# Kernel optimization log

Hardware: AMD Instinct MI355X
Metric: run time of the kernel (lower is better)

Reference implementation:

```python
import jax, jax.numpy as jnp
import numpy as np

NUM_TASKS = 150
ACT_DIM = 4
ENC_DIM = 256
EMB_DIM = 32
HEAD_HID = 128
B, H, W = 256, 128, 128


def _conv(x, w, b):
    # x: NCHW, w: OIHW, stride 2, padding 1 (torch Conv2d semantics)
    y = jax.lax.conv_general_dilated(x, w, window_strides=(2, 2),
                                     padding=((1, 1), (1, 1)),
                                     dimension_numbers=('NCHW', 'OIHW', 'NCHW'))
    return y + b[None, :, None, None]


def setup_inputs() -> dict:
    key = jax.random.key(0)
    ks = iter(jax.random.split(key, 32))
    s = 0.05
    d = {
        'images': jax.random.normal(next(ks), (B, 3, H, W), jnp.float32),
        'proprioception': jax.random.normal(next(ks), (B, 7), jnp.float32),
        'task_ids': jax.random.randint(next(ks), (B,), 0, NUM_TASKS, jnp.int32),
        # vision encoder convs (OIHW)
        'c1_w': jax.random.normal(next(ks), (64, 3, 3, 3), jnp.float32) * s,
        'c1_b': jnp.zeros((64,), jnp.float32),
        'c2_w': jax.random.normal(next(ks), (128, 64, 3, 3), jnp.float32) * s,
        'c2_b': jnp.zeros((128,), jnp.float32),
        'c3_w': jax.random.normal(next(ks), (256, 128, 3, 3), jnp.float32) * s,
        'c3_b': jnp.zeros((256,), jnp.float32),
        # proprioception encoder (weights stored as [in, out])
        'p1_w': jax.random.normal(next(ks), (7, 64), jnp.float32) * s,
        'p1_b': jnp.zeros((64,), jnp.float32),
        'p2_w': jax.random.normal(next(ks), (64, 64), jnp.float32) * s,
        'p2_b': jnp.zeros((64,), jnp.float32),
        # shared-encoder fusion MLP (320 -> 256 -> 256)
        'f1_w': jax.random.normal(next(ks), (256 + 64, ENC_DIM), jnp.float32) * s,
        'f1_b': jnp.zeros((ENC_DIM,), jnp.float32),
        'f2_w': jax.random.normal(next(ks), (ENC_DIM, ENC_DIM), jnp.float32) * s,
        'f2_b': jnp.zeros((ENC_DIM,), jnp.float32),
        # task embedding table
        'task_emb': jax.random.normal(next(ks), (NUM_TASKS, EMB_DIM), jnp.float32) * s,
        # policy-level fusion (288 -> 256), dropout is identity at inference
        'g_w': jax.random.normal(next(ks), (ENC_DIM + EMB_DIM, ENC_DIM), jnp.float32) * s,
        'g_b': jnp.zeros((ENC_DIM,), jnp.float32),
        # stacked task-specific heads [num_tasks, in, out]
        'h1_w': jax.random.normal(next(ks), (NUM_TASKS, ENC_DIM, HEAD_HID), jnp.float32) * s,
        'h1_b': jnp.zeros((NUM_TASKS, HEAD_HID), jnp.float32),
        'h2_w': jax.random.normal(next(ks), (NUM_TASKS, HEAD_HID, HEAD_HID), jnp.float32) * s,
        'h2_b': jnp.zeros((NUM_TASKS, HEAD_HID), jnp.float32),
        'h3_w': jax.random.normal(next(ks), (NUM_TASKS, HEAD_HID, ACT_DIM), jnp.float32) * s,
        'h3_b': jnp.zeros((NUM_TASKS, ACT_DIM), jnp.float32),
    }
    return d


def reference(images, proprioception, task_ids,
              c1_w, c1_b, c2_w, c2_b, c3_w, c3_b,
              p1_w, p1_b, p2_w, p2_b,
              f1_w, f1_b, f2_w, f2_b,
              task_emb, g_w, g_b,
              h1_w, h1_b, h2_w, h2_b, h3_w, h3_b):
    relu = jax.nn.relu
    # vision encoder: 3 strided convs + global avg pool (AdaptiveAvgPool2d(1,1))
    v = relu(_conv(images, c1_w, c1_b))
    v = relu(_conv(v, c2_w, c2_b))
    v = relu(_conv(v, c3_w, c3_b))
    v = jnp.mean(v, axis=(2, 3))                      # [B, 256]
    # proprioception encoder (no final ReLU)
    p = relu(proprioception @ p1_w + p1_b) @ p2_w + p2_b  # [B, 64]
    # shared fusion
    f = relu(jnp.concatenate([v, p], axis=1) @ f1_w + f1_b)
    f = relu(f @ f2_w + f2_b)                         # [B, 256]
    # task embedding + policy fusion (dropout = identity in eval)
    e = task_emb[task_ids]                            # [B, 32]
    z = relu(jnp.concatenate([f, e], axis=1) @ g_w + g_b)  # [B, 256]
    # routed task heads: gather per-sample expert params, batched matmuls
    a = relu(jnp.einsum('bd,bdh->bh', z, h1_w[task_ids]) + h1_b[task_ids])
    a = relu(jnp.einsum('bd,bdh->bh', a, h2_w[task_ids]) + h2_b[task_ids])
    a = jnp.einsum('bd,bdh->bh', a, h3_w[task_ids]) + h3_b[task_ids]  # [B, 4]
    return a
```

## Files before the change

kernel.cpp:

```cpp
#include <hip/hip_runtime.h>
#include <hip/hip_bf16.h>

#define DIV_UP(a,b) (((a)+(b)-1)/(b))

typedef __attribute__((ext_vector_type(8))) short short8;
typedef __attribute__((ext_vector_type(4))) float f32x4;

__device__ __forceinline__ ushort bf16_bits(float x) {
    return __builtin_bit_cast(ushort, __float2bfloat16(x));
}

__device__ __forceinline__ void gload_lds16(const ushort* g, ushort* l) {
    __builtin_amdgcn_global_load_lds(
        (const __attribute__((address_space(1))) void*)g,
        (__attribute__((address_space(3))) void*)l, 16, 0, 0);
}

__global__ __launch_bounds__(256) void halo_zero_kernel(
    uint4* __restrict__ act1, uint4* __restrict__ act2,
    float4* __restrict__ vbuf) {
    const int b = blockIdx.x, tid = threadIdx.x;
    const uint4 z = {0u, 0u, 0u, 0u};
    uint4* a1 = act1 + (size_t)b * 33800;
    for (int i = tid; i < 520; i += 256) a1[i] = z;
    for (int i = tid; i < 512; i += 256) {
        int r = (i >> 3) + 1;
        a1[r * 520 + (i & 7)] = z;
    }
    uint4* a2 = act2 + (size_t)b * 17424;
    for (int i = tid; i < 528; i += 256) a2[i] = z;
    for (int i = tid; i < 512; i += 256) {
        int r = (i >> 4) + 1;
        a2[r * 528 + (i & 15)] = z;
    }
    int idx = b * 256 + tid;
    float4 zf = {0.f, 0.f, 0.f, 0.f};
    if (idx < 16384) vbuf[idx] = zf;
}

__global__ void repack_w1_kernel(const float* __restrict__ src,
                                 __hip_bfloat16* __restrict__ dst) {
    int t = blockIdx.x * blockDim.x + threadIdx.x;
    if (t >= 2048) return;
    int k  = t & 31;
    int oc = t >> 5;
    dst[t] = (k < 27) ? __float2bfloat16(src[oc * 27 + k])
                      : __float2bfloat16(0.f);
}

__global__ void repack_w_kernel(const float* __restrict__ src,
                                __hip_bfloat16* __restrict__ dst, int O, int C) {
    int t = blockIdx.x * blockDim.x + threadIdx.x;
    if (t >= O * C * 9) return;
    int e   = t & 7;
    int r   = t >> 3;
    int n   = r % O;
    int q   = r / O;
    int SEG = C >> 3;
    int sg  = q % SEG;
    int tap = q / SEG;
    dst[t] = __float2bfloat16(src[(n * C + sg * 8 + e) * 9 + tap]);
}

__global__ __launch_bounds__(256) void conv1_mfma_kernel(
    const float* __restrict__ in,
    const __hip_bfloat16* __restrict__ wB,
    const float* __restrict__ bias,
    __hip_bfloat16* __restrict__ out) {
    const int tid  = threadIdx.x;
    const int lane = tid & 63;
    const int wv   = tid >> 6;
    const int l15  = lane & 15;
    const int quad = lane >> 4;
    const int tile = blockIdx.x;
    const int b    = blockIdx.y;
    const int oh0  = tile << 2;

    __shared__ __align__(16) char smem[30208];
    float*  sx = (float*)smem;
    ushort* Al = (ushort*)(smem + 13824);

    const float* ip  = in + (size_t)b * 3 * 128 * 128;
    const int    ih0 = 2 * oh0 - 1;

#pragma unroll
    for (int it = 0; it < 4; ++it) {
        int e = (it << 8) + tid;
        if (e < 864) {
            int q = e >> 5, k = e & 31;
            int c = q / 9, r = q - c * 9;
            int row = ih0 + r;
            if (row < 0) row = 0;
            gload_lds16((const ushort*)(ip + c * 16384 + row * 128 + k * 4),
                        (ushort*)smem + (size_t)e * 8);
        }
    }
    __syncthreads();

    const int px = tid, ohl = px >> 6, ow = px & 63;
    union { uint4 u4[4]; ushort us[32]; } rowv;
#pragma unroll
    for (int c = 0; c < 3; ++c)
#pragma unroll
        for (int kh = 0; kh < 3; ++kh) {
            const bool rok = (ih0 + 2 * ohl + kh) >= 0;
            const float* srow = sx + (c * 9 + 2 * ohl + kh) * 128;
#pragma unroll
            for (int kw = 0; kw < 3; ++kw) {
                int iw = 2 * ow + kw - 1;
                bool ok = rok && (iw >= 0);
                float x = srow[iw < 0 ? 0 : iw];
                rowv.us[c * 9 + kh * 3 + kw] = bf16_bits(ok ? x : 0.f);
            }
        }
#pragma unroll
    for (int k = 27; k < 32; ++k) rowv.us[k] = 0;
#pragma unroll
    for (int q = 0; q < 4; ++q)
        *(uint4*)(Al + px * 32 + (((q ^ (px >> 1)) & 3) << 3)) = rowv.u4[q];

    short8 af[4], bf[4];
#pragma unroll
    for (int i = 0; i < 4; ++i)
        af[i] = __builtin_bit_cast(short8,
            *(const uint4*)(wB + ((i * 16 + l15) * 32 + quad * 8)));

    __syncthreads();

#pragma unroll
    for (int j = 0; j < 4; ++j) {
        int p = wv * 64 + j * 16 + l15;
        bf[j] = __builtin_bit_cast(short8,
            *(const uint4*)(Al + p * 32 + (((quad ^ (p >> 1)) & 3) << 3)));
    }
    f32x4 acc[4][4];
#pragma unroll
    for (int i = 0; i < 4; ++i)
#pragma unroll
        for (int j = 0; j < 4; ++j)
            acc[i][j] = __builtin_amdgcn_mfma_f32_16x16x32_bf16(
                af[i], bf[j], (f32x4){0.f, 0.f, 0.f, 0.f}, 0, 0, 0);

    float4 bv[4];
#pragma unroll
    for (int i = 0; i < 4; ++i)
        bv[i] = *(const float4*)(bias + i * 16 + quad * 4);

    __hip_bfloat16* ob = out + (((size_t)b * 65 + oh0 + 1) * 65 + 1) * 64;
#pragma unroll
    for (int j = 0; j < 4; ++j) {
        const int oww = j * 16 + l15;
        __hip_bfloat16* op = ob + ((size_t)(wv * 65) + oww) * 64 + quad * 4;
#pragma unroll
        for (int i = 0; i < 4; ++i) {
            union { uint2 u2; ushort us[4]; } pk;
#pragma unroll
            for (int r = 0; r < 4; ++r)
                pk.us[r] = bf16_bits(
                    fmaxf(acc[i][j][r] + ((const float*)&bv[i])[r], 0.f));
            *(uint2*)(op + i * 16) = pk.u2;
        }
    }
}

__global__ __launch_bounds__(256, 2) void conv2_gemm_kernel(
    const __hip_bfloat16* __restrict__ act,
    const __hip_bfloat16* __restrict__ wtB,
    const float* __restrict__ bias,
    __hip_bfloat16* __restrict__ out) {
    const int tid  = threadIdx.x;
    const int lane = tid & 63;
    const int w    = tid >> 6;
    const int l15  = lane & 15;
    const int quad = lane >> 4;
    const int per  = gridDim.x >> 3;
    const int Mt   = (blockIdx.x & 7) * per + (blockIdx.x >> 3);
    const int bimg = Mt >> 3;
    const int oh0  = (Mt & 7) << 2;

    __shared__ __align__(16) char smem[77824];
    ushort* As = (ushort*)smem;
    ushort* Cs = (ushort*)smem;

    f32x4 acc[4][4];
#pragma unroll
    for (int i = 0; i < 4; ++i)
#pragma unroll
        for (int j = 0; j < 4; ++j) acc[i][j] = (f32x4){0.f, 0.f, 0.f, 0.f};

    const int wm = (w & 1) << 6;
    const int wn = (w >> 1) << 6;
    const size_t abase = ((size_t)(bimg * 65 + 2 * oh0)) * 65 * 64;
    const ushort* ap = (const ushort*)act;

#pragma unroll
    for (int it = 0; it < 19; ++it) {
        int c  = (it << 8) + tid;
        int p  = c >> 3;
        int t  = c & 7;
        int h  = t >> 2;
        int ss = (t & 3) ^ ((p >> 1) & 3);
        gload_lds16(ap + abase + (size_t)p * 64 + h * 32 + ss * 8,
                    As + (size_t)c * 8);
    }
    __syncthreads();

    for (int h = 0; h < 2; ++h) {
#pragma unroll
        for (int tap = 0; tap < 9; ++tap) {
            const int kh = tap / 3, kw = tap - kh * 3;
            short8 af[4], bf[4];
#pragma unroll
            for (int i = 0; i < 4; ++i) {
                int ml = wm + i * 16 + l15;
                int p  = ((ml >> 5) * 2 + kh) * 65 + ((ml & 31) * 2 + kw);
                af[i] = __builtin_bit_cast(short8,
                    *(const uint4*)(As + p * 64 + h * 32 +
                                    (((quad ^ (p >> 1)) & 3) << 3)));
            }
#pragma unroll
            for (int j = 0; j < 4; ++j)
                bf[j] = __builtin_bit_cast(short8,
                    *(const uint4*)(wtB +
                        ((size_t)((tap * 8 + h * 4 + quad) * 128) +
                         wn + j * 16 + l15) * 8));
#pragma unroll
            for (int i = 0; i < 4; ++i)
#pragma unroll
                for (int j = 0; j < 4; ++j)
                    acc[i][j] = __builtin_amdgcn_mfma_f32_16x16x32_bf16(
                        af[i], bf[j], acc[i][j], 0, 0, 0);
        }
    }

    __syncthreads();
#pragma unroll
    for (int j = 0; j < 4; ++j) {
        int n = wn + j * 16 + l15;
        float bv = bias[n];
#pragma unroll
        for (int i = 0; i < 4; ++i)
#pragma unroll
            for (int r = 0; r < 4; ++r) {
                int ml = wm + i * 16 + quad * 4 + r;
                Cs[ml * 132 + n] = bf16_bits(fmaxf(acc[i][j][r] + bv, 0.f));
            }
    }
    __syncthreads();
#pragma unroll
    for (int q = 0; q < 16; ++q) {
        int c   = tid + 256 * q;
        int row = c >> 5;
        int off = c & 31;
        uint2 val = *(const uint2*)(Cs + row * 132 + off * 4);
        int m  = (Mt << 7) + row;
        int b  = m >> 10;
        int rr = m & 1023;
        int oh = rr >> 5;
        int ow = rr & 31;
        size_t pix = ((size_t)(b * 33 + oh + 1) * 33 + (ow + 1));
        *(uint2*)(out + pix * 128 + off * 4) = val;
    }
}

__global__ __launch_bounds__(256, 2) void conv3_gemm_pool_kernel(
    const __hip_bfloat16* __restrict__ act,
    const __hip_bfloat16* __restrict__ wtB,
    const float* __restrict__ bias,
    float* __restrict__ v ) {
    const int tid  = threadIdx.x;
    const int lane = tid & 63;
    const int w    = tid >> 6;
    const int l15  = lane & 15;
    const int quad = lane >> 4;
    const int per  = gridDim.x >> 3;
    const int Mt   = (blockIdx.x & 7) * per + (blockIdx.x >> 3);
    const int bimg = Mt >> 2;
    const int oh0  = (Mt & 3) << 2;

    __shared__ __align__(16) char smem[77824];
    ushort* As   = (ushort*)smem;
    float*  sred = (float*)smem;

    f32x4 acc[4][4];
#pragma unroll
    for (int i = 0; i < 4; ++i)
#pragma unroll
        for (int j = 0; j < 4; ++j) acc[i][j] = (f32x4){0.f, 0.f, 0.f, 0.f};

    const int wn = w << 6;
    const size_t abase = ((size_t)(bimg * 33 + 2 * oh0)) * 33 * 128;
    const ushort* ap = (const ushort*)act;

#pragma unroll
    for (int it = 0; it < 19; ++it) {
        int c  = (it << 8) + tid;
        int p  = c >> 4;
        int t  = c & 15;
        int h  = t >> 3;
        int ss = (t & 7) ^ ((p >> 1) & 7);
        gload_lds16(ap + abase + (size_t)p * 128 + h * 64 + ss * 8,
                    As + (size_t)c * 8);
    }
    __syncthreads();

    for (int h = 0; h < 2; ++h) {
#pragma unroll 1
        for (int tap = 0; tap < 9; ++tap) {
            const int kh = tap / 3, kw = tap - kh * 3;
#pragma unroll
            for (int ks = 0; ks < 2; ++ks) {
                short8 af[4], bf[4];
                const int sl = ks * 4 + quad;
#pragma unroll
                for (int i = 0; i < 4; ++i) {
                    int p = (i * 2 + kh) * 33 + l15 * 2 + kw;
                    af[i] = __builtin_bit_cast(short8,
                        *(const uint4*)(As + p * 128 + h * 64 +
                                        (((sl ^ (p >> 1)) & 7) << 3)));
                }
#pragma unroll
                for (int j = 0; j < 4; ++j)
                    bf[j] = __builtin_bit_cast(short8,
                        *(const uint4*)(wtB +
                            ((size_t)((tap * 16 + h * 8 + sl) * 256) +
                             wn + j * 16 + l15) * 8));
#pragma unroll
                for (int i = 0; i < 4; ++i)
#pragma unroll
                    for (int j = 0; j < 4; ++j)
                        acc[i][j] = __builtin_amdgcn_mfma_f32_16x16x32_bf16(
                            af[i], bf[j], acc[i][j], 0, 0, 0);
            }
        }
    }

    float s4[4];
#pragma unroll
    for (int j = 0; j < 4; ++j) {
        float bv = bias[wn + j * 16 + l15];
        float s = 0.f;
#pragma unroll
        for (int i = 0; i < 4; ++i)
#pragma unroll
            for (int r = 0; r < 4; ++r)
                s += fmaxf(acc[i][j][r] + bv, 0.f);
        s += __shfl_xor(s, 16, 64);
        s += __shfl_xor(s, 32, 64);
        s4[j] = s;
    }
    __syncthreads();
    if (quad == 0) {
#pragma unroll
        for (int j = 0; j < 4; ++j) sred[wn + j * 16 + l15] = s4[j];
    }
    __syncthreads();
    atomicAdd(v + (size_t)bimg * 256 + tid, sred[tid] * (1.f / 256.f));
}

template<int N, int K, int S, bool RELU>
__device__ __forceinline__ void gemv_stage(const float* __restrict__ w,
                                           const float* __restrict__ bias,
                                           const float* in, float* outv,
                                           float4* red4, int tid) {
    constexpr int G = N / 4;
    constexpr int CHK = K / S;
    static_assert(G * S == 256 && CHK * S == K, "stage shape");
    const int g = tid % G, s = tid / G;
    const float4* wp = (const float4*)w;
    float4 a; a.x = a.y = a.z = a.w = 0.f;
    const int k0 = s * CHK;
#pragma unroll 8
    for (int i = 0; i < CHK; ++i) {
        float x = in[k0 + i];
        float4 wv = wp[(size_t)(k0 + i) * G + g];
        a.x = fmaf(x, wv.x, a.x);
        a.y = fmaf(x, wv.y, a.y);
        a.z = fmaf(x, wv.z, a.z);
        a.w = fmaf(x, wv.w, a.w);
    }
    red4[tid] = a;
    __syncthreads();
    if (tid < N) {
        int gg = tid >> 2, e = tid & 3;
        float vv = bias[tid];
#pragma unroll
        for (int ss = 0; ss < S; ++ss) {
            const float* rp = (const float*)(red4 + ss * G + gg);
            vv += rp[e];
        }
        if (RELU) vv = fmaxf(vv, 0.f);
        outv[tid] = vv;
    }
    __syncthreads();
}

__global__ __launch_bounds__(256) void tail_kernel(
    const float* __restrict__ prop, const int* __restrict__ task_ids,
    const float* __restrict__ p1_w, const float* __restrict__ p1_b,
    const float* __restrict__ p2_w, const float* __restrict__ p2_b,
    const float* __restrict__ v,
    const float* __restrict__ f1_w, const float* __restrict__ f1_b,
    const float* __restrict__ f2_w, const float* __restrict__ f2_b,
    const float* __restrict__ task_emb,
    const float* __restrict__ g_w, const float* __restrict__ g_b,
    const float* __restrict__ h1_w, const float* __restrict__ h1_b,
    const float* __restrict__ h2_w, const float* __restrict__ h2_b,
    const float* __restrict__ h3_w, const float* __restrict__ h3_b,
    float* __restrict__ out) {
    const int b   = blockIdx.x;
    const int tid = threadIdx.x;
    const int t   = task_ids[b];
    __shared__ float sa[320];
    __shared__ float sb[288];
    __shared__ float sph[64];
    __shared__ float4 red4[256];

    sa[tid] = (tid < 256) ? v[(size_t)b * 256 + tid] : 0.f;
    if (tid < 64) {
        float h = p1_b[tid];
#pragma unroll
        for (int k = 0; k < 7; ++k) h = fmaf(prop[b * 7 + k], p1_w[k * 64 + tid], h);
        sph[tid] = fmaxf(h, 0.f);
    }
    __syncthreads();
    gemv_stage<64, 64, 16, false>(p2_w, p2_b, sph, sa + 256, red4, tid);
    gemv_stage<256, 320, 4, true>(f1_w, f1_b, sa, sb, red4, tid);
    gemv_stage<256, 256, 4, true>(f2_w, f2_b, sb, sa, red4, tid);
    if (tid < 32) sa[256 + tid] = task_emb[t * 32 + tid];
    __syncthreads();
    gemv_stage<256, 288, 4, true>(g_w, g_b, sa, sb, red4, tid);
    gemv_stage<128, 256, 8, true>(h1_w + (size_t)t * 32768, h1_b + t * 128,
                                  sb, sa, red4, tid);
    gemv_stage<128, 128, 8, true>(h2_w + (size_t)t * 16384, h2_b + t * 128,
                                  sa, sb, red4, tid);
    if (tid < 128) {
        float4 wv = ((const float4*)(h3_w + (size_t)t * 512))[tid];
        float x = sb[tid];
        float r0 = x * wv.x, r1 = x * wv.y, r2 = x * wv.z, r3 = x * wv.w;
#pragma unroll
        for (int off = 1; off < 64; off <<= 1) {
            r0 += __shfl_xor(r0, off, 64);
            r1 += __shfl_xor(r1, off, 64);
            r2 += __shfl_xor(r2, off, 64);
            r3 += __shfl_xor(r3, off, 64);
        }
        if ((tid & 63) == 0) {
            float4 rv; rv.x = r0; rv.y = r1; rv.z = r2; rv.w = r3;
            red4[tid >> 6] = rv;
        }
    }
    __syncthreads();
    if (tid < 4) {
        const float* ra = (const float*)(red4 + 0);
        const float* rb = (const float*)(red4 + 1);
        out[b * 4 + tid] = ra[tid] + rb[tid] + h3_b[t * 4 + tid];
    }
}

extern "C" void kernel_launch(void* const* d_in, const int* in_sizes, int n_in,
                              void* d_out, int out_size, void* d_ws, size_t ws_size,
                              hipStream_t stream) {
    (void)in_sizes; (void)n_in; (void)out_size;
    const float* images   = (const float*)d_in[0];
    const float* prop     = (const float*)d_in[1];
    const int*   task_ids = (const int*)d_in[2];
    const float* c1_w = (const float*)d_in[3];
    const float* c1_b = (const float*)d_in[4];
    const float* c2_w = (const float*)d_in[5];
    const float* c2_b = (const float*)d_in[6];
    const float* c3_w = (const float*)d_in[7];
    const float* c3_b = (const float*)d_in[8];
    const float* p1_w = (const float*)d_in[9];
    const float* p1_b = (const float*)d_in[10];
    const float* p2_w = (const float*)d_in[11];
    const float* p2_b = (const float*)d_in[12];
    const float* f1_w = (const float*)d_in[13];
    const float* f1_b = (const float*)d_in[14];
    const float* f2_w = (const float*)d_in[15];
    const float* f2_b = (const float*)d_in[16];
    const float* temb = (const float*)d_in[17];
    const float* g_w  = (const float*)d_in[18];
    const float* g_b  = (const float*)d_in[19];
    const float* h1_w = (const float*)d_in[20];
    const float* h1_b = (const float*)d_in[21];
    const float* h2_w = (const float*)d_in[22];
    const float* h2_b = (const float*)d_in[23];
    const float* h3_w = (const float*)d_in[24];
    const float* h3_b = (const float*)d_in[25];
    float* out = (float*)d_out;

    const size_t per_img = (size_t)65 * 65 * 64 * 2 + (size_t)33 * 33 * 128 * 2;
    const size_t fixed   = (size_t)256 * 256 * 4 + 1728 * 4 +
                           (size_t)73728 * 2 + (size_t)294912 * 2 + 4096;
    int CHI = 64;
    if (ws_size >= fixed + per_img * 256) CHI = 256;
    else if (ws_size >= fixed + per_img * 128) CHI = 128;

    char* ws = (char*)d_ws;
    size_t off = 0;
    auto alloc = [&](size_t bytes) {
        void* p = ws + off;
        off += (bytes + 255) & ~(size_t)255;
        return p;
    };
    __hip_bfloat16* act1 = (__hip_bfloat16*)alloc((size_t)CHI * 65 * 65 * 64 * 2);
    __hip_bfloat16* act2 = (__hip_bfloat16*)alloc((size_t)CHI * 33 * 33 * 128 * 2);
    float*          vbuf = (float*)alloc((size_t)256 * 256 * 4);
    __hip_bfloat16* w1b  = (__hip_bfloat16*)alloc((size_t)2048 * 2);
    __hip_bfloat16* w2t  = (__hip_bfloat16*)alloc((size_t)73728 * 2);
    __hip_bfloat16* w3t  = (__hip_bfloat16*)alloc((size_t)294912 * 2);

    halo_zero_kernel<<<dim3(CHI), 256, 0, stream>>>(
        (uint4*)act1, (uint4*)act2, (float4*)vbuf);
    repack_w1_kernel<<<8, 256, 0, stream>>>(c1_w, w1b);
    repack_w_kernel<<<DIV_UP(73728, 256), 256, 0, stream>>>(c2_w, w2t, 128, 64);
    repack_w_kernel<<<DIV_UP(294912, 256), 256, 0, stream>>>(c3_w, w3t, 256, 128);

    for (int c0 = 0; c0 < 256; c0 += CHI) {
        const float* img_c = images + (size_t)c0 * 3 * 128 * 128;
        conv1_mfma_kernel<<<dim3(16, CHI), dim3(256), 0, stream>>>(
            img_c, w1b, c1_b, act1);
        conv2_gemm_kernel<<<dim3(CHI * 8), 256, 0, stream>>>(
            act1, w2t, c2_b, act2);
        conv3_gemm_pool_kernel<<<dim3(CHI * 4), 256, 0, stream>>>(
            act2, w3t, c3_b, vbuf + (size_t)c0 * 256);
    }
    tail_kernel<<<256, 256, 0, stream>>>(prop, task_ids, p1_w, p1_b, p2_w, p2_b,
                                         vbuf, f1_w, f1_b, f2_w, f2_b, temb,
                                         g_w, g_b, h1_w, h1_b, h2_w, h2_b,
                                         h3_w, h3_b, out);
}
```

Measured before the change: 334.4 us.

## Make conv2/conv3 persistent with double-buffered LDS tile prefetch

Conv2 and conv3 GEMM kernels now launch a fixed 256 blocks, each looping over k consecutive M-tiles. Each block double-buffers the activation tile in LDS, prefetching the next tile with async global-to-LDS loads while computing the current one. Conv2 also swaps the A/B operand roles so it can write output straight from registers instead of staging through LDS. Conv3 issues pool atomics directly from shuffled partial sums. The doubled LDS footprint limits each CU to one block, and the hand-written vmcnt waits depend on exact load counts.

```diff
diff --git a/kernel.cpp b/kernel.cpp
--- a/kernel.cpp
+++ b/kernel.cpp
@@ -163,199 +163,230 @@
     }
 }
 
-__global__ __launch_bounds__(256, 2) void conv2_gemm_kernel(
+__global__ __launch_bounds__(256) void conv2_gemm_kernel(
     const __hip_bfloat16* __restrict__ act,
     const __hip_bfloat16* __restrict__ wtB,
     const float* __restrict__ bias,
-    __hip_bfloat16* __restrict__ out) {
+    __hip_bfloat16* __restrict__ out, int k ) {
     const int tid  = threadIdx.x;
     const int lane = tid & 63;
     const int w    = tid >> 6;
     const int l15  = lane & 15;
     const int quad = lane >> 4;
-    const int per  = gridDim.x >> 3;
-    const int Mt   = (blockIdx.x & 7) * per + (blockIdx.x >> 3);
-    const int bimg = Mt >> 3;
-    const int oh0  = (Mt & 7) << 2;
-
-    __shared__ __align__(16) char smem[77824];
+    const int wm   = (w & 1) << 6;
+    const int wn   = (w >> 1) << 6;
+    const int Mt0  = blockIdx.x * k;
+
+    __shared__ __align__(16) char smem[155648];
     ushort* As = (ushort*)smem;
-    ushort* Cs = (ushort*)smem;
-
-    f32x4 acc[4][4];
+    const ushort* ap = (const ushort*)act;
+
+    float4 bv[4];
 #pragma unroll
     for (int i = 0; i < 4; ++i)
-#pragma unroll
-        for (int j = 0; j < 4; ++j) acc[i][j] = (f32x4){0.f, 0.f, 0.f, 0.f};
-
-    const int wm = (w & 1) << 6;
-    const int wn = (w >> 1) << 6;
-    const size_t abase = ((size_t)(bimg * 65 + 2 * oh0)) * 65 * 64;
-    const ushort* ap = (const ushort*)act;
-
-#pragma unroll
-    for (int it = 0; it < 19; ++it) {
-        int c  = (it << 8) + tid;
-        int p  = c >> 3;
-        int t  = c & 7;
-        int h  = t >> 2;
-        int ss = (t & 3) ^ ((p >> 1) & 3);
-        gload_lds16(ap + abase + (size_t)p * 64 + h * 32 + ss * 8,
-                    As + (size_t)c * 8);
-    }
-    __syncthreads();
-
-    for (int h = 0; h < 2; ++h) {
-#pragma unroll
-        for (int tap = 0; tap < 9; ++tap) {
-            const int kh = tap / 3, kw = tap - kh * 3;
-            short8 af[4], bf[4];
+        bv[i] = *(const float4*)(bias + wm + i * 16 + quad * 4);
+
+    auto stage = [&](int t) {
+        const int Mt = Mt0 + t;
+        const int bimg = Mt >> 3, oh0 = (Mt & 7) << 2;
+        const size_t abase = ((size_t)(bimg * 65 + 2 * oh0)) * 65 * 64;
+        ushort* buf = As + (size_t)(t & 1) * 38912;
+#pragma unroll
+        for (int it = 0; it < 19; ++it) {
+            int cc = (it << 8) + tid;
+            int p  = cc >> 3, q8 = cc & 7;
+            int hh = q8 >> 2;
+            int ss = (q8 & 3) ^ ((p >> 1) & 3);
+            gload_lds16(ap + abase + (size_t)p * 64 + hh * 32 + ss * 8,
+                        buf + (size_t)cc * 8);
+        }
+    };
+
+    stage(0);
+    for (int t = 0; t < k; ++t) {
+        if (t + 1 < k) {
+            stage(t + 1);
+            if (t == 0) asm volatile("s_waitcnt vmcnt(19)" ::: "memory");
+            else        asm volatile("s_waitcnt vmcnt(35)" ::: "memory");
+        } else {
+            asm volatile("s_waitcnt vmcnt(0)" ::: "memory");
+        }
+        __builtin_amdgcn_sched_barrier(0);
+        __builtin_amdgcn_s_barrier();
+        __builtin_amdgcn_sched_barrier(0);
+
+        const ushort* buf = As + (size_t)(t & 1) * 38912;
+        const int Mt = Mt0 + t;
+        const int bimg = Mt >> 3, oh0 = (Mt & 7) << 2;
+
+        f32x4 acc[4][4];
+#pragma unroll
+        for (int i = 0; i < 4; ++i)
+#pragma unroll
+            for (int j = 0; j < 4; ++j) acc[i][j] = (f32x4){0.f, 0.f, 0.f, 0.f};
+
+        for (int h = 0; h < 2; ++h) {
+#pragma unroll
+            for (int tap = 0; tap < 9; ++tap) {
+                const int kh = tap / 3, kw = tap - kh * 3;
+                short8 af[4], bf[4];
+#pragma unroll
+                for (int i = 0; i < 4; ++i)
+                    af[i] = __builtin_bit_cast(short8,
+                        *(const uint4*)(wtB +
+                            ((size_t)((tap * 8 + h * 4 + quad) * 128) +
+                             wm + i * 16 + l15) * 8));
+#pragma unroll
+                for (int j = 0; j < 4; ++j) {
+                    int px = wn + j * 16 + l15;
+                    int p  = ((px >> 5) * 2 + kh) * 65 + ((px & 31) * 2 + kw);
+                    bf[j] = __builtin_bit_cast(short8,
+                        *(const uint4*)(buf + p * 64 + h * 32 +
+                                        (((quad ^ (p >> 1)) & 3) << 3)));
+                }
+#pragma unroll
+                for (int i = 0; i < 4; ++i)
+#pragma unroll
+                    for (int j = 0; j < 4; ++j)
+                        acc[i][j] = __builtin_amdgcn_mfma_f32_16x16x32_bf16(
+                            af[i], bf[j], acc[i][j], 0, 0, 0);
+            }
+        }
+
+        __hip_bfloat16* ob = out;
+#pragma unroll
+        for (int j = 0; j < 4; ++j) {
+            int px  = wn + j * 16 + l15;
+            int ohl = px >> 5, ow = px & 31;
+            __hip_bfloat16* op = ob +
+                (((size_t)(bimg * 33) + oh0 + ohl + 1) * 33 + (ow + 1)) * 128 +
+                wm + quad * 4;
 #pragma unroll
             for (int i = 0; i < 4; ++i) {
-                int ml = wm + i * 16 + l15;
-                int p  = ((ml >> 5) * 2 + kh) * 65 + ((ml & 31) * 2 + kw);
-                af[i] = __builtin_bit_cast(short8,
-                    *(const uint4*)(As + p * 64 + h * 32 +
-                                    (((quad ^ (p >> 1)) & 3) << 3)));
+                union { uint2 u2; ushort us[4]; } pk;
+#pragma unroll
+                for (int r = 0; r < 4; ++r)
+                    pk.us[r] = bf16_bits(
+                        fmaxf(acc[i][j][r] + ((const float*)&bv[i])[r], 0.f));
+                *(uint2*)(op + i * 16) = pk.u2;
             }
-#pragma unroll
-            for (int j = 0; j < 4; ++j)
-                bf[j] = __builtin_bit_cast(short8,
-                    *(const uint4*)(wtB +
-                        ((size_t)((tap * 8 + h * 4 + quad) * 128) +
-                         wn + j * 16 + l15) * 8));
-#pragma unroll
-            for (int i = 0; i < 4; ++i)
-#pragma unroll
-                for (int j = 0; j < 4; ++j)
-                    acc[i][j] = __builtin_amdgcn_mfma_f32_16x16x32_bf16(
-                        af[i], bf[j], acc[i][j], 0, 0, 0);
-        }
-    }
-
-    __syncthreads();
-#pragma unroll
-    for (int j = 0; j < 4; ++j) {
-        int n = wn + j * 16 + l15;
-        float bv = bias[n];
-#pragma unroll
-        for (int i = 0; i < 4; ++i)
-#pragma unroll
-            for (int r = 0; r < 4; ++r) {
-                int ml = wm + i * 16 + quad * 4 + r;
-                Cs[ml * 132 + n] = bf16_bits(fmaxf(acc[i][j][r] + bv, 0.f));
-            }
-    }
-    __syncthreads();
-#pragma unroll
-    for (int q = 0; q < 16; ++q) {
-        int c   = tid + 256 * q;
-        int row = c >> 5;
-        int off = c & 31;
-        uint2 val = *(const uint2*)(Cs + row * 132 + off * 4);
-        int m  = (Mt << 7) + row;
-        int b  = m >> 10;
-        int rr = m & 1023;
-        int oh = rr >> 5;
-        int ow = rr & 31;
-        size_t pix = ((size_t)(b * 33 + oh + 1) * 33 + (ow + 1));
-        *(uint2*)(out + pix * 128 + off * 4) = val;
-    }
-}
-
-__global__ __launch_bounds__(256, 2) void conv3_gemm_pool_kernel(
+        }
+
+        asm volatile("s_waitcnt lgkmcnt(0)" ::: "memory");
+        __builtin_amdgcn_sched_barrier(0);
+        __builtin_amdgcn_s_barrier();
+        __builtin_amdgcn_sched_barrier(0);
+    }
+}
+
+__global__ __launch_bounds__(256) void conv3_gemm_pool_kernel(
     const __hip_bfloat16* __restrict__ act,
     const __hip_bfloat16* __restrict__ wtB,
     const float* __restrict__ bias,
-    float* __restrict__ v ) {
+    float* __restrict__ v , int k) {
     const int tid  = threadIdx.x;
     const int lane = tid & 63;
     const int w    = tid >> 6;
     const int l15  = lane & 15;
     const int quad = lane >> 4;
-    const int per  = gridDim.x >> 3;
-    const int Mt   = (blockIdx.x & 7) * per + (blockIdx.x >> 3);
-    const int bimg = Mt >> 2;
-    const int oh0  = (Mt & 3) << 2;
-
-    __shared__ __align__(16) char smem[77824];
-    ushort* As   = (ushort*)smem;
-    float*  sred = (float*)smem;
-
-    f32x4 acc[4][4];
-#pragma unroll
-    for (int i = 0; i < 4; ++i)
-#pragma unroll
-        for (int j = 0; j < 4; ++j) acc[i][j] = (f32x4){0.f, 0.f, 0.f, 0.f};
-
-    const int wn = w << 6;
-    const size_t abase = ((size_t)(bimg * 33 + 2 * oh0)) * 33 * 128;
+    const int wn   = w << 6;
+    const int Mt0  = blockIdx.x * k;
+
+    __shared__ __align__(16) char smem[155648];
+    ushort* As = (ushort*)smem;
     const ushort* ap = (const ushort*)act;
 
-#pragma unroll
-    for (int it = 0; it < 19; ++it) {
-        int c  = (it << 8) + tid;
-        int p  = c >> 4;
-        int t  = c & 15;
-        int h  = t >> 3;
-        int ss = (t & 7) ^ ((p >> 1) & 7);
-        gload_lds16(ap + abase + (size_t)p * 128 + h * 64 + ss * 8,
-                    As + (size_t)c * 8);
-    }
-    __syncthreads();
-
-    for (int h = 0; h < 2; ++h) {
+    auto stage = [&](int t) {
+        const int Mt = Mt0 + t;
+        const int bimg = Mt >> 2, oh0 = (Mt & 3) << 2;
+        const size_t abase = ((size_t)(bimg * 33 + 2 * oh0)) * 33 * 128;
+        ushort* buf = As + (size_t)(t & 1) * 38912;
+#pragma unroll
+        for (int it = 0; it < 19; ++it) {
+            int cc = (it << 8) + tid;
+            int p  = cc >> 4, q16 = cc & 15;
+            int hh = q16 >> 3;
+            int ss = (q16 & 7) ^ ((p >> 1) & 7);
+            gload_lds16(ap + abase + (size_t)p * 128 + hh * 64 + ss * 8,
+                        buf + (size_t)cc * 8);
+        }
+    };
+
+    stage(0);
+    for (int t = 0; t < k; ++t) {
+        if (t + 1 < k) {
+            stage(t + 1);
+            if (t == 0) asm volatile("s_waitcnt vmcnt(19)" ::: "memory");
+            else        asm volatile("s_waitcnt vmcnt(35)" ::: "memory");
+        } else {
+            asm volatile("s_waitcnt vmcnt(0)" ::: "memory");
+        }
+        __builtin_amdgcn_sched_barrier(0);
+        __builtin_amdgcn_s_barrier();
+        __builtin_amdgcn_sched_barrier(0);
+
+        const ushort* buf = As + (size_t)(t & 1) * 38912;
+        const int Mt = Mt0 + t;
+        const int bimg = Mt >> 2;
+
+        f32x4 acc[4][4];
+#pragma unroll
+        for (int i = 0; i < 4; ++i)
+#pragma unroll
+            for (int j = 0; j < 4; ++j) acc[i][j] = (f32x4){0.f, 0.f, 0.f, 0.f};
+
+        for (int h = 0; h < 2; ++h) {
 #pragma unroll 1
-        for (int tap = 0; tap < 9; ++tap) {
-            const int kh = tap / 3, kw = tap - kh * 3;
-#pragma unroll
-            for (int ks = 0; ks < 2; ++ks) {
-                short8 af[4], bf[4];
-                const int sl = ks * 4 + quad;
-#pragma unroll
-                for (int i = 0; i < 4; ++i) {
-                    int p = (i * 2 + kh) * 33 + l15 * 2 + kw;
-                    af[i] = __builtin_bit_cast(short8,
-                        *(const uint4*)(As + p * 128 + h * 64 +
-                                        (((sl ^ (p >> 1)) & 7) << 3)));
+            for (int tap = 0; tap < 9; ++tap) {
+                const int kh = tap / 3, kw = tap - kh * 3;
+#pragma unroll
+                for (int ks = 0; ks < 2; ++ks) {
+                    short8 af[4], bf[4];
+                    const int sl = ks * 4 + quad;
+#pragma unroll
+                    for (int i = 0; i < 4; ++i) {
+                        int p = (i * 2 + kh) * 33 + l15 * 2 + kw;
+                        af[i] = __builtin_bit_cast(short8,
+                            *(const uint4*)(buf + p * 128 + h * 64 +
+                                            (((sl ^ (p >> 1)) & 7) << 3)));
+                    }
+#pragma unroll
+                    for (int j = 0; j < 4; ++j)
+                        bf[j] = __builtin_bit_cast(short8,
+                            *(const uint4*)(wtB +
+                                ((size_t)((tap * 16 + h * 8 + sl) * 256) +
+                                 wn + j * 16 + l15) * 8));
+#pragma unroll
+                    for (int i = 0; i < 4; ++i)
+#pragma unroll
+                        for (int j = 0; j < 4; ++j)
+                            acc[i][j] = __builtin_amdgcn_mfma_f32_16x16x32_bf16(
+                                af[i], bf[j], acc[i][j], 0, 0, 0);
                 }
-#pragma unroll
-                for (int j = 0; j < 4; ++j)
-                    bf[j] = __builtin_bit_cast(short8,
-                        *(const uint4*)(wtB +
-                            ((size_t)((tap * 16 + h * 8 + sl) * 256) +
-                             wn + j * 16 + l15) * 8));
-#pragma unroll
-                for (int i = 0; i < 4; ++i)
-#pragma unroll
-                    for (int j = 0; j < 4; ++j)
-                        acc[i][j] = __builtin_amdgcn_mfma_f32_16x16x32_bf16(
-                            af[i], bf[j], acc[i][j], 0, 0, 0);
             }
         }
-    }
-
-    float s4[4];
-#pragma unroll
-    for (int j = 0; j < 4; ++j) {
-        float bv = bias[wn + j * 16 + l15];
-        float s = 0.f;
-#pragma unroll
-        for (int i = 0; i < 4; ++i)
-#pragma unroll
-            for (int r = 0; r < 4; ++r)
-                s += fmaxf(acc[i][j][r] + bv, 0.f);
-        s += __shfl_xor(s, 16, 64);
-        s += __shfl_xor(s, 32, 64);
-        s4[j] = s;
-    }
-    __syncthreads();
-    if (quad == 0) {
-#pragma unroll
-        for (int j = 0; j < 4; ++j) sred[wn + j * 16 + l15] = s4[j];
-    }
-    __syncthreads();
-    atomicAdd(v + (size_t)bimg * 256 + tid, sred[tid] * (1.f / 256.f));
+
+#pragma unroll
+        for (int j = 0; j < 4; ++j) {
+            float bvs = bias[wn + j * 16 + l15];
+            float s = 0.f;
+#pragma unroll
+            for (int i = 0; i < 4; ++i)
+#pragma unroll
+                for (int r = 0; r < 4; ++r)
+                    s += fmaxf(acc[i][j][r] + bvs, 0.f);
+            s += __shfl_xor(s, 16, 64);
+            s += __shfl_xor(s, 32, 64);
+            if (quad == 0)
+                atomicAdd(v + (size_t)bimg * 256 + wn + j * 16 + l15,
+                          s * (1.f / 256.f));
+        }
+
+        asm volatile("s_waitcnt lgkmcnt(0)" ::: "memory");
+        __builtin_amdgcn_sched_barrier(0);
+        __builtin_amdgcn_s_barrier();
+        __builtin_amdgcn_sched_barrier(0);
+    }
 }
 
 template<int N, int K, int S, bool RELU>
@@ -521,10 +552,10 @@
         const float* img_c = images + (size_t)c0 * 3 * 128 * 128;
         conv1_mfma_kernel<<<dim3(16, CHI), dim3(256), 0, stream>>>(
             img_c, w1b, c1_b, act1);
-        conv2_gemm_kernel<<<dim3(CHI * 8), 256, 0, stream>>>(
-            act1, w2t, c2_b, act2);
-        conv3_gemm_pool_kernel<<<dim3(CHI * 4), 256, 0, stream>>>(
-            act2, w3t, c3_b, vbuf + (size_t)c0 * 256);
+        conv2_gemm_kernel<<<dim3(256), 256, 0, stream>>>(
+            act1, w2t, c2_b, act2, CHI * 8 / 256);
+        conv3_gemm_pool_kernel<<<dim3(256), 256, 0, stream>>>(
+            act2, w3t, c3_b, vbuf + (size_t)c0 * 256, CHI * 4 / 256);
     }
     tail_kernel<<<256, 256, 0, stream>>>(prop, task_ids, p1_w, p1_b, p2_w, p2_b,
                                          vbuf, f1_w, f1_b, f2_w, f2_b, temb,
```

Result: slower. 432.1 us (+29.2%).
